# Performance work log

Measured on AMD Instinct MI355X. Metric: run time of the kernel, lower is better.

## Reference

```python
import jax, jax.numpy as jnp
import numpy as np


def setup_inputs() -> dict:
    key = jax.random.key(0)
    k1, k2, k3, k4, k5 = jax.random.split(key, 5)
    B, T, N, F, H = 32, 12, 512, 64, 64
    cat_x = jax.random.normal(k1, (B, T, N, F), dtype=jnp.float32)
    # Linear params (stored as [in, out]; torch stores [out, in] and does x @ W.T)
    lim = 1.0 / np.sqrt(F)
    Wq = jax.random.uniform(k2, (F, H), jnp.float32, -lim, lim)
    bq = jax.random.uniform(k3, (H,), jnp.float32, -lim, lim)
    Wk = jax.random.uniform(k4, (F, H), jnp.float32, -lim, lim)
    bk = jax.random.uniform(k5, (H,), jnp.float32, -lim, lim)
    return {"cat_x": cat_x, "Wq": Wq, "bq": bq, "Wk": Wk, "bk": bk, "tau": 4}


def reference(cat_x, Wq, bq, Wk, bk, tau):
    # cat_x: [B, T, N, F]
    q = cat_x @ Wq + bq  # [B, T, N, H]
    k = cat_x @ Wk + bk  # [B, T, N, H]
    qf = jnp.fft.rfft(q, axis=-1)  # [B, T, N, Fr]
    kf = jnp.fft.rfft(k, axis=-1)  # [B, T, N, Fr]
    # Vectorized over the original Python loop over i (query time step):
    # res[b, i, j, n, :] = qf[b, i, n, :] * conj(kf[b, j, n, :])
    res = qf[:, :, None, :, :] * jnp.conj(kf)[:, None, :, :, :]  # [B, Ti, Tj, N, Fr]
    corr = jnp.fft.irfft(res, axis=-1)  # [B, Ti, Tj, N, H] (H even -> exact round trip)
    # mean over batch, then hidden (last), then nodes == mean over (B, N, H)
    score_set = jnp.mean(corr, axis=(0, 3, 4))  # [Ti, Tj]
    scores, indices = jax.lax.top_k(score_set, tau)
    return scores, indices
```

## Files before the change

kernel.cpp:

```cpp
#include <hip/hip_runtime.h>

#define BB 32
#define TT 12
#define NN 512
#define FF 64
#define HH 64
#define NBLK 8
#define NCHUNK (NN / NBLK)
#define GRID (BB * NCHUNK)
#define NSHADOW 16


__global__ __launch_bounds__(256, 8) void fft_sel_main(
    const float* __restrict__ x,
    const float* __restrict__ Wq, const float* __restrict__ bq,
    const float* __restrict__ Wk, const float* __restrict__ bk,
    float* __restrict__ S)
{
    __shared__ __align__(16) float wq_s[FF];
    __shared__ __align__(16) float wk_s[FF];
    __shared__ float bsum[2];
    __shared__ float sq[TT][NBLK];
    __shared__ float sk[TT][NBLK];

    const int tid = threadIdx.x;

    if (tid < FF) {
        const float* p = Wq + tid * HH;
        float a = 0.f;
        #pragma unroll
        for (int h = 0; h < HH; ++h) a += p[h];
        wq_s[tid] = a;
    } else if (tid < 2 * FF) {
        const float* p = Wk + (tid - FF) * HH;
        float a = 0.f;
        #pragma unroll
        for (int h = 0; h < HH; ++h) a += p[h];
        wk_s[tid - FF] = a;
    } else if (tid == 2 * FF) {
        float a = 0.f;
        #pragma unroll
        for (int h = 0; h < HH; ++h) a += bq[h];
        bsum[0] = a;
    } else if (tid == 2 * FF + 1) {
        float a = 0.f;
        #pragma unroll
        for (int h = 0; h < HH; ++h) a += bk[h];
        bsum[1] = a;
    }
    __syncthreads();

    const int q = tid & 15;
    const float4 wqv = *(const float4*)(wq_s + 4 * q);
    const float4 wkv = *(const float4*)(wk_s + 4 * q);
    const float  bqs = bsum[0];
    const float  bks = bsum[1];

    const int b  = blockIdx.x >> 6;
    const int n0 = (blockIdx.x & (NCHUNK - 1)) * NBLK;

    #pragma unroll
    for (int it = 0; it < (TT * NBLK * 16) / 256; ++it) {
        const int s   = it * 256 + tid;
        const int row = s >> 4;
        const int t   = row >> 3;
        const int nl  = row & (NBLK - 1);
        const float4 v = *(const float4*)(x +
            (((size_t)b * TT + t) * NN + (n0 + nl)) * FF + q * 4);
        float pq = v.x * wqv.x + v.y * wqv.y + v.z * wqv.z + v.w * wqv.w;
        float pk = v.x * wkv.x + v.y * wkv.y + v.z * wkv.z + v.w * wkv.w;
        #pragma unroll
        for (int off = 1; off < 16; off <<= 1) {
            pq += __shfl_xor(pq, off);
            pk += __shfl_xor(pk, off);
        }
        if (q == 0) {
            sq[t][nl] = pq + bqs;
            sk[t][nl] = pk + bks;
        }
    }
    __syncthreads();

    if (tid < TT * TT) {
        const int i = tid / TT;
        const int j = tid % TT;
        float acc = 0.f;
        #pragma unroll
        for (int nl = 0; nl < NBLK; ++nl) acc += sq[i][nl] * sk[j][nl];
        atomicAdd(&S[(blockIdx.x & (NSHADOW - 1)) * (TT * TT) + tid], acc);
    }
}

__global__ __launch_bounds__(256) void fft_sel_final(
    const float* __restrict__ Sg, float* __restrict__ out)
{
    __shared__ float S[TT * TT];
    const int tid = threadIdx.x;
    if (tid < TT * TT) {
        const float scale = 1.0f / ((float)BB * (float)NN * (float)HH);
        float a = 0.f;
        #pragma unroll
        for (int c = 0; c < NSHADOW; ++c) a += Sg[c * TT * TT + tid];
        S[tid] = a * scale;
    }
    __syncthreads();
    if (tid < TT) {
        const int i = tid;
        float v[TT];
        bool used[TT];
        #pragma unroll
        for (int j = 0; j < TT; ++j) { v[j] = S[i * TT + j]; used[j] = false; }
        #pragma unroll
        for (int s4 = 0; s4 < 4; ++s4) {
            float best = -INFINITY;
            int bi = 0;
            for (int j = 0; j < TT; ++j) {
                if (!used[j] && v[j] > best) { best = v[j]; bi = j; }
            }
            used[bi] = true;
            out[i * 4 + s4]          = best;
            out[TT * 4 + i * 4 + s4] = (float)bi;
        }
    }
}

extern "C" void kernel_launch(void* const* d_in, const int* in_sizes, int n_in,
                              void* d_out, int out_size, void* d_ws, size_t ws_size,
                              hipStream_t stream) {
    const float* x  = (const float*)d_in[0];
    const float* Wq = (const float*)d_in[1];
    const float* bq = (const float*)d_in[2];
    const float* Wk = (const float*)d_in[3];
    const float* bk = (const float*)d_in[4];
    float* S = (float*)d_ws;

    fft_sel_main<<<GRID, 256, 0, stream>>>(x, Wq, bq, Wk, bk, S);
    fft_sel_final<<<1, 256, 0, stream>>>(S, (float*)d_out);
}
```

Measured before the change: 99.53 us.

## Fuse final top-k into main kernel via last-block counter; widen per-thread loads

Removes the separate finalize kernel launch. Each block bumps an atomic counter stored after the partial-sum shadow buffers, and the last block to finish reduces the shadow copies and does the per-row top-4 selection. It also has each thread load 8 contiguous floats (two float4) instead of 4, which cuts the shuffle reduction from 4 to 3 steps and halves the loop iterations. The cost is a threadfence and an extra counter atomic in every block. Correctness depends on the workspace counter starting at zero (or at a 0xAA poison pattern) on every call.

```diff
diff --git a/kernel.cpp b/kernel.cpp
--- a/kernel.cpp
+++ b/kernel.cpp
@@ -10,18 +10,22 @@
 #define GRID (BB * NCHUNK)
 #define NSHADOW 16
 
+#define WS_CNT (NSHADOW * TT * TT)
 
-__global__ __launch_bounds__(256, 8) void fft_sel_main(
+__global__ __launch_bounds__(256, 8) void fft_sel_fused(
     const float* __restrict__ x,
     const float* __restrict__ Wq, const float* __restrict__ bq,
     const float* __restrict__ Wk, const float* __restrict__ bk,
-    float* __restrict__ S)
+    float* __restrict__ S,
+    float* __restrict__ out)
 {
     __shared__ __align__(16) float wq_s[FF];
     __shared__ __align__(16) float wk_s[FF];
     __shared__ float bsum[2];
     __shared__ float sq[TT][NBLK];
     __shared__ float sk[TT][NBLK];
+    __shared__ float Sf[TT * TT];
+    __shared__ unsigned last_flag;
 
     const int tid = threadIdx.x;
 
@@ -50,9 +54,11 @@
     }
     __syncthreads();
 
-    const int q = tid & 15;
-    const float4 wqv = *(const float4*)(wq_s + 4 * q);
-    const float4 wkv = *(const float4*)(wk_s + 4 * q);
+    const int q8 = tid & 7;
+    const float4 wq0 = *(const float4*)(wq_s + 8 * q8);
+    const float4 wq1 = *(const float4*)(wq_s + 8 * q8 + 4);
+    const float4 wk0 = *(const float4*)(wk_s + 8 * q8);
+    const float4 wk1 = *(const float4*)(wk_s + 8 * q8 + 4);
     const float  bqs = bsum[0];
     const float  bks = bsum[1];
 
@@ -60,21 +66,22 @@
     const int n0 = (blockIdx.x & (NCHUNK - 1)) * NBLK;
 
     #pragma unroll
-    for (int it = 0; it < (TT * NBLK * 16) / 256; ++it) {
+    for (int it = 0; it < 3; ++it) {
         const int s   = it * 256 + tid;
-        const int row = s >> 4;
+        const int row = s >> 3;
         const int t   = row >> 3;
         const int nl  = row & (NBLK - 1);
-        const float4 v = *(const float4*)(x +
-            (((size_t)b * TT + t) * NN + (n0 + nl)) * FF + q * 4);
-        float pq = v.x * wqv.x + v.y * wqv.y + v.z * wqv.z + v.w * wqv.w;
-        float pk = v.x * wkv.x + v.y * wkv.y + v.z * wkv.z + v.w * wkv.w;
-        #pragma unroll
-        for (int off = 1; off < 16; off <<= 1) {
-            pq += __shfl_xor(pq, off);
-            pk += __shfl_xor(pk, off);
-        }
-        if (q == 0) {
+        const float* rp = x +
+            (((size_t)b * TT + t) * NN + (n0 + nl)) * FF + q8 * 8;
+        const float4 v0 = *(const float4*)(rp);
+        const float4 v1 = *(const float4*)(rp + 4);
+        float pq = v0.x * wq0.x + v0.y * wq0.y + v0.z * wq0.z + v0.w * wq0.w
+                 + v1.x * wq1.x + v1.y * wq1.y + v1.z * wq1.z + v1.w * wq1.w;
+        float pk = v0.x * wk0.x + v0.y * wk0.y + v0.z * wk0.z + v0.w * wk0.w
+                 + v1.x * wk1.x + v1.y * wk1.y + v1.z * wk1.z + v1.w * wk1.w;
+        pq += __shfl_xor(pq, 1); pq += __shfl_xor(pq, 2); pq += __shfl_xor(pq, 4);
+        pk += __shfl_xor(pk, 1); pk += __shfl_xor(pk, 2); pk += __shfl_xor(pk, 4);
+        if (q8 == 0) {
             sq[t][nl] = pq + bqs;
             sk[t][nl] = pk + bks;
         }
@@ -89,19 +96,28 @@
         for (int nl = 0; nl < NBLK; ++nl) acc += sq[i][nl] * sk[j][nl];
         atomicAdd(&S[(blockIdx.x & (NSHADOW - 1)) * (TT * TT) + tid], acc);
     }
-}
 
-__global__ __launch_bounds__(256) void fft_sel_final(
-    const float* __restrict__ Sg, float* __restrict__ out)
-{
-    __shared__ float S[TT * TT];
-    const int tid = threadIdx.x;
+    __threadfence();
+    __syncthreads();
+    if (tid == 0) {
+        unsigned* cnt = (unsigned*)(S + WS_CNT);
+        unsigned old = __hip_atomic_fetch_add(cnt, 1u, __ATOMIC_ACQ_REL,
+                                              __HIP_MEMORY_SCOPE_AGENT);
+        last_flag = (old == (unsigned)(GRID - 1)) ||
+                    (old == 0xAAAAAAAAu + (unsigned)(GRID - 1));
+    }
+    __syncthreads();
+    if (!last_flag) return;
+
+    __threadfence();
     if (tid < TT * TT) {
         const float scale = 1.0f / ((float)BB * (float)NN * (float)HH);
         float a = 0.f;
         #pragma unroll
-        for (int c = 0; c < NSHADOW; ++c) a += Sg[c * TT * TT + tid];
-        S[tid] = a * scale;
+        for (int c = 0; c < NSHADOW; ++c)
+            a += __hip_atomic_load(&S[c * TT * TT + tid], __ATOMIC_RELAXED,
+                                   __HIP_MEMORY_SCOPE_AGENT);
+        Sf[tid] = a * scale;
     }
     __syncthreads();
     if (tid < TT) {
@@ -109,7 +125,7 @@
         float v[TT];
         bool used[TT];
         #pragma unroll
-        for (int j = 0; j < TT; ++j) { v[j] = S[i * TT + j]; used[j] = false; }
+        for (int j = 0; j < TT; ++j) { v[j] = Sf[i * TT + j]; used[j] = false; }
         #pragma unroll
         for (int s4 = 0; s4 < 4; ++s4) {
             float best = -INFINITY;
@@ -134,6 +150,5 @@
     const float* bk = (const float*)d_in[4];
     float* S = (float*)d_ws;
 
-    fft_sel_main<<<GRID, 256, 0, stream>>>(x, Wq, bq, Wk, bk, S);
-    fft_sel_final<<<1, 256, 0, stream>>>(S, (float*)d_out);
+    fft_sel_fused<<<GRID, 256, 0, stream>>>(x, Wq, bq, Wk, bk, S, (float*)d_out);
 }
```

New measurement: 305.8 us. 207% more time.
